# Optimization experiments

Measured on AMD Instinct MI355X. Metric: run time of the kernel, lower is better.

Reference implementation:

```python
import jax, jax.numpy as jnp
import numpy as np

B, L, D, H = 4, 2048, 1024, 16
DH = D // H


def setup_inputs() -> dict:
    key = jax.random.key(0)
    ks = jax.random.split(key, 16)
    s = 1.0 / np.sqrt(D)
    return {
        "query": jax.random.normal(ks[0], (B, L, D), jnp.float32),
        "key_": jax.random.normal(ks[1], (B, L, D), jnp.float32),
        "value": jax.random.normal(ks[2], (B, L, D), jnp.float32),
        "mask": jax.random.randint(ks[3], (B, L), 0, 2, jnp.int32),
        "Wq": jax.random.normal(ks[4], (D, D), jnp.float32) * s,
        "bq": jnp.zeros((D,), jnp.float32),
        "Wk": jax.random.normal(ks[5], (D, D), jnp.float32) * s,
        "bk": jnp.zeros((D,), jnp.float32),
        "Wv": jax.random.normal(ks[6], (D, D), jnp.float32) * s,
        "bv": jnp.zeros((D,), jnp.float32),
        "Wo": jax.random.normal(ks[7], (D, D), jnp.float32) * s,
        "bo": jnp.zeros((D,), jnp.float32),
        "gamma": jnp.ones((D,), jnp.float32),
        "beta": jnp.zeros((D,), jnp.float32),
    }


def reference(query, key_, value, mask, Wq, bq, Wk, bk, Wv, bv, Wo, bo, gamma, beta):
    old_query = query
    # projections (Linear: x @ W^T + b)
    q = query @ Wq.T + bq            # [B,L,D]
    k = key_ @ Wk.T + bk
    v = value @ Wv.T + bv
    # split heads -> [B,H,L,DH]
    q = q.reshape(B, L, H, DH).transpose(0, 2, 1, 3)
    k = k.reshape(B, L, H, DH).transpose(0, 2, 1, 3)
    v = v.reshape(B, L, H, DH).transpose(0, 2, 1, 3)
    scores = jnp.einsum("bhqd,bhkd->bhqk", q, k) / jnp.sqrt(jnp.float32(DH))
    m = mask[:, None, None, :]        # [B,1,1,L]
    scores = jnp.where(m == 0, jnp.float32(-1e9), scores)
    attn = jax.nn.softmax(scores, axis=-1)
    out = jnp.einsum("bhqk,bhkd->bhqd", attn, v)
    out = out.transpose(0, 2, 1, 3).reshape(B, L, D)
    out = out @ Wo.T + bo
    # dropout is identity in eval; residual + layernorm (eps=1e-5)
    x = out + old_query
    mu = jnp.mean(x, axis=-1, keepdims=True)
    var = jnp.var(x, axis=-1, keepdims=True)
    return (x - mu) / jnp.sqrt(var + 1e-5) * gamma + beta
```

## Files before the change

kernel.cpp:

```cpp
#include <hip/hip_runtime.h>
#include <hip/hip_bf16.h>

typedef __attribute__((ext_vector_type(4))) float f32x4;
typedef __attribute__((ext_vector_type(16))) float f32x16;
typedef __attribute__((ext_vector_type(2))) unsigned int u32x2;
typedef __attribute__((ext_vector_type(4))) unsigned int u32x4;
typedef __attribute__((ext_vector_type(8))) __bf16 bf16x8;

__device__ inline unsigned short f2bf(float x) {
    return __builtin_bit_cast(unsigned short, (__bf16)x);
}
__device__ inline unsigned int pack2(float lo, float hi) {
    return (unsigned int)f2bf(lo) | ((unsigned int)f2bf(hi) << 16);
}
__device__ inline u32x4 cvt8(const float* __restrict__ p) {
    f32x4 a = *(const f32x4*)p;
    f32x4 b = *(const f32x4*)(p + 4);
    u32x4 r;
    r[0] = pack2(a[0], a[1]);
    r[1] = pack2(a[2], a[3]);
    r[2] = pack2(b[0], b[1]);
    r[3] = pack2(b[2], b[3]);
    return r;
}
__device__ inline bf16x8 ldfrag(const unsigned short* p) {
    u32x4 t = *(const u32x4*)p;
    return __builtin_bit_cast(bf16x8, t);
}

__global__ __launch_bounds__(256) void cvt_bf16(
    const float* __restrict__ src, unsigned short* __restrict__ dst, int n8)
{
    for (int i = blockIdx.x * 256 + threadIdx.x; i < n8; i += gridDim.x * 256)
        *(u32x4*)(dst + (size_t)i * 8) = cvt8(src + (size_t)i * 8);
}
__global__ __launch_bounds__(256) void cvt_w3(
    const float* __restrict__ wq, const float* __restrict__ wk,
    const float* __restrict__ wv, unsigned short* __restrict__ dst)
{
    const float* s = blockIdx.y == 0 ? wq : (blockIdx.y == 1 ? wk : wv);
    unsigned short* d = dst + (size_t)blockIdx.y * 1048576;
    const int i = blockIdx.x * 256 + threadIdx.x;
    *(u32x4*)(d + (size_t)i * 8) = cvt8(s + (size_t)i * 8);
}

template<int MODE>
__global__ __launch_bounds__(256) void gemm_bt(
    const unsigned short* __restrict__ A, const unsigned short* __restrict__ Bw,
    const float* __restrict__ bias, const float* __restrict__ resid,
    void* __restrict__ Cp, float alpha)
{
    __shared__ unsigned short Al[2][128][32];
    __shared__ unsigned short Bl[2][128][32];
    const int tid = threadIdx.x;
    const int lane = tid & 63, w = tid >> 6;
    const int wr = w >> 1, wc = w & 1;
    const int m0 = blockIdx.x * 128, n0 = blockIdx.y * 128;
    const int fr = lane & 15, fq = lane >> 4;

    f32x4 acc[4][4] = {};

    auto stage = [&](int p, int k0) {
#pragma unroll
        for (int j = 0; j < 2; ++j) {
            const int f = (w * 2 + j) * 512 + lane * 8;
            const int r = f >> 5, c = f & 31;
            __builtin_amdgcn_global_load_lds(
                (const __attribute__((address_space(1))) void*)(A + (size_t)(m0 + r) * 1024 + k0 + c),
                (__attribute__((address_space(3))) void*)(&Al[p][0][0] + (w * 2 + j) * 512),
                16, 0, 0);
            __builtin_amdgcn_global_load_lds(
                (const __attribute__((address_space(1))) void*)(Bw + (size_t)(n0 + r) * 1024 + k0 + c),
                (__attribute__((address_space(3))) void*)(&Bl[p][0][0] + (w * 2 + j) * 512),
                16, 0, 0);
        }
    };

    stage(0, 0);
    __syncthreads();

    for (int k0 = 0; k0 < 1024; k0 += 32) {
        const int p = (k0 >> 5) & 1;
        if (k0 + 32 < 1024) stage(p ^ 1, k0 + 32);

        bf16x8 af[4], bfv[4];
#pragma unroll
        for (int mt = 0; mt < 4; ++mt)
            af[mt] = ldfrag(&Al[p][wr * 64 + mt * 16 + fr][8 * fq]);
#pragma unroll
        for (int nt = 0; nt < 4; ++nt)
            bfv[nt] = ldfrag(&Bl[p][wc * 64 + nt * 16 + fr][8 * fq]);
#pragma unroll
        for (int mt = 0; mt < 4; ++mt)
#pragma unroll
            for (int nt = 0; nt < 4; ++nt)
                acc[mt][nt] = __builtin_amdgcn_mfma_f32_16x16x32_bf16(af[mt], bfv[nt], acc[mt][nt], 0, 0, 0);
        __syncthreads();
    }

#pragma unroll
    for (int mt = 0; mt < 4; ++mt) {
#pragma unroll
        for (int nt = 0; nt < 4; ++nt) {
            const int col = n0 + wc * 64 + nt * 16 + fr;
            const float bb = bias[col];
            const int row0 = m0 + wr * 64 + mt * 16 + fq * 4;
            if (MODE == 2) {
                float v0 = acc[mt][nt][0] + bb, v1 = acc[mt][nt][1] + bb;
                float v2 = acc[mt][nt][2] + bb, v3 = acc[mt][nt][3] + bb;
                const int bb_ = row0 >> 11, key = row0 & 2047;
                const int key2 = (key & ~12) | ((key & 4) << 1) | ((key & 8) >> 1);
                const size_t idx = ((size_t)bb_ * 1024 + col) * 2048 + key2;
                u32x2 pv;
                pv[0] = pack2(v0, v1);
                pv[1] = pack2(v2, v3);
                *(u32x2*)((unsigned short*)Cp + idx) = pv;
            } else {
#pragma unroll
                for (int r = 0; r < 4; ++r) {
                    const size_t idx = (size_t)(row0 + r) * 1024 + col;
                    float v = (acc[mt][nt][r] + bb) * alpha;
                    if (MODE == 1) ((float*)Cp)[idx] = v + resid[idx];
                    else           ((unsigned short*)Cp)[idx] = f2bf(v);
                }
            }
        }
    }
}

__global__ __launch_bounds__(256, 2) void attn_fwd(
    const unsigned short* __restrict__ Q, const unsigned short* __restrict__ K,
    const unsigned short* __restrict__ Vt_g, const int* __restrict__ mask,
    unsigned short* __restrict__ O)
{
    __shared__ unsigned short Kl[2][64][64];
    __shared__ unsigned short Vl[2][64][64];
    __shared__ unsigned short mlb[2][64];
    const int tid = threadIdx.x, lane = tid & 63, w = tid >> 6;
    const int l31 = lane & 31, hi = lane >> 5;
    const int qb = blockIdx.y >> 3;
    const int bh = ((blockIdx.y & 7) << 3) | blockIdx.x;
    const int q0 = qb * 256;
    const int b = bh >> 4;
    const size_t rowbase = (size_t)b * 2048;
    const int hoff = (bh & 15) * 64;
    const size_t vbase = (size_t)bh * 64 * 2048;

    const u32x4 onesu = {0x3F803F80u, 0x3F803F80u, 0x3F803F80u, 0x3F803F80u};
    const bf16x8 vones = __builtin_bit_cast(bf16x8, onesu);

    const int sw0 = (((l31) ^ (l31 >> 3)) & 7) << 3;
    const int sw1 = (((l31) ^ ((l31 >> 3) + 4)) & 7) << 3;

    bf16x8 aq[2][4];
#pragma unroll
    for (int a = 0; a < 2; ++a) {
        const unsigned short* qp = Q + (rowbase + q0 + w * 64 + a * 32 + l31) * 1024 + hoff + hi * 8;
#pragma unroll
        for (int kk = 0; kk < 4; ++kk) aq[a][kk] = ldfrag(qp + kk * 16);
    }
    f32x16 o[2][2] = {};
    f32x16 os[2] = {};

    int srow[2], scol[2];
#pragma unroll
    for (int i = 0; i < 2; ++i) {
        int e = (i * 256 + tid) * 8;
        srow[i] = e >> 6;
        scol[i] = e & 63;
    }

    u32x4 kpre[2], vpre[2];
    int mpre = 0;
#pragma unroll
    for (int i = 0; i < 2; ++i) {
        kpre[i] = *(const u32x4*)(K + (rowbase + srow[i]) * 1024 + hoff + scol[i]);
        vpre[i] = *(const u32x4*)(Vt_g + vbase + (size_t)srow[i] * 2048 + scol[i]);
    }
    if (tid < 64) mpre = mask[rowbase + tid];

    for (int kb = 0, it = 0; kb < 2048; kb += 64, ++it) {
        const int p = it & 1;
#pragma unroll
        for (int i = 0; i < 2; ++i) {
            const int cs = scol[i] ^ (((srow[i] ^ (srow[i] >> 3)) & 7) << 3);
            *(u32x4*)&Kl[p][srow[i]][cs] = kpre[i];
            *(u32x4*)&Vl[p][srow[i]][cs] = vpre[i];
        }
        if (tid < 64) mlb[p][tid] = f2bf(mpre == 0 ? -30000.0f : 0.0f);
        if (kb + 64 < 2048) {
#pragma unroll
            for (int i = 0; i < 2; ++i) {
                kpre[i] = *(const u32x4*)(K + (rowbase + kb + 64 + srow[i]) * 1024 + hoff + scol[i]);
                vpre[i] = *(const u32x4*)(Vt_g + vbase + (size_t)srow[i] * 2048 + kb + 64 + scol[i]);
            }
            if (tid < 64) mpre = mask[rowbase + kb + 64 + tid];
        }
        __syncthreads();

#pragma unroll
        for (int t = 0; t < 2; ++t) {
            const int swt = t ? sw1 : sw0;
            const unsigned int mv = (hi == 0) ? (unsigned int)mlb[p][t * 32 + l31] : 0u;
            const u32x4 mfu = {mv, 0u, 0u, 0u};
            const bf16x8 kfm = __builtin_bit_cast(bf16x8, mfu);

            f32x16 z0 = {}, z1 = {};
            __builtin_amdgcn_s_setprio(1);
            z0 = __builtin_amdgcn_mfma_f32_32x32x16_bf16(kfm, vones, z0, 0, 0, 0);
            z1 = __builtin_amdgcn_mfma_f32_32x32x16_bf16(kfm, vones, z1, 0, 0, 0);
#pragma unroll
            for (int kk = 0; kk < 4; ++kk) {
                bf16x8 kf = ldfrag(&Kl[p][t * 32 + l31][(kk * 16 + hi * 8) ^ swt]);
                z0 = __builtin_amdgcn_mfma_f32_32x32x16_bf16(kf, aq[0][kk], z0, 0, 0, 0);
                z1 = __builtin_amdgcn_mfma_f32_32x32x16_bf16(kf, aq[1][kk], z1, 0, 0, 0);
            }
            __builtin_amdgcn_s_setprio(0);

            unsigned int pk[2][4][2];
#pragma unroll
            for (int g = 0; g < 4; ++g) {
                {
                    float p0 = __builtin_amdgcn_exp2f(z0[g * 4 + 0]);
                    float p1 = __builtin_amdgcn_exp2f(z0[g * 4 + 1]);
                    float p2 = __builtin_amdgcn_exp2f(z0[g * 4 + 2]);
                    float p3 = __builtin_amdgcn_exp2f(z0[g * 4 + 3]);
                    pk[0][g][0] = pack2(p0, p1);
                    pk[0][g][1] = pack2(p2, p3);
                }
                {
                    float p0 = __builtin_amdgcn_exp2f(z1[g * 4 + 0]);
                    float p1 = __builtin_amdgcn_exp2f(z1[g * 4 + 1]);
                    float p2 = __builtin_amdgcn_exp2f(z1[g * 4 + 2]);
                    float p3 = __builtin_amdgcn_exp2f(z1[g * 4 + 3]);
                    pk[1][g][0] = pack2(p0, p1);
                    pk[1][g][1] = pack2(p2, p3);
                }
            }

#pragma unroll
            for (int half = 0; half < 2; ++half) {
                const int c = t * 2 + half, G = half * 2;
                u32x4 fu0 = {pk[0][G][0], pk[0][G][1], pk[0][G + 1][0], pk[0][G + 1][1]};
                u32x4 fu1 = {pk[1][G][0], pk[1][G][1], pk[1][G + 1][0], pk[1][G + 1][1]};
                bf16x8 pf0 = __builtin_bit_cast(bf16x8, fu0);
                bf16x8 pf1 = __builtin_bit_cast(bf16x8, fu1);
                __builtin_amdgcn_s_setprio(1);
#pragma unroll
                for (int dt = 0; dt < 2; ++dt) {
                    const int swd = dt ? sw1 : sw0;
                    bf16x8 vb = ldfrag(&Vl[p][dt * 32 + l31][(c * 16 + hi * 8) ^ swd]);
                    o[0][dt] = __builtin_amdgcn_mfma_f32_32x32x16_bf16(pf0, vb, o[0][dt], 0, 0, 0);
                    o[1][dt] = __builtin_amdgcn_mfma_f32_32x32x16_bf16(pf1, vb, o[1][dt], 0, 0, 0);
                }
                os[0] = __builtin_amdgcn_mfma_f32_32x32x16_bf16(pf0, vones, os[0], 0, 0, 0);
                os[1] = __builtin_amdgcn_mfma_f32_32x32x16_bf16(pf1, vones, os[1], 0, 0, 0);
                __builtin_amdgcn_s_setprio(0);
            }
        }
    }

#pragma unroll
    for (int a = 0; a < 2; ++a)
#pragma unroll
        for (int g = 0; g < 4; ++g)
#pragma unroll
            for (int j = 0; j < 4; ++j) {
                const float inv = 1.0f / os[a][g * 4 + j];
                const size_t row = rowbase + q0 + w * 64 + a * 32 + g * 8 + hi * 4 + j;
#pragma unroll
                for (int dt = 0; dt < 2; ++dt)
                    O[row * 1024 + hoff + dt * 32 + l31] = f2bf(o[a][dt][g * 4 + j] * inv);
            }
}

__global__ __launch_bounds__(256) void ln_inplace(
    float* __restrict__ X, const float* __restrict__ gamma, const float* __restrict__ beta)
{
    __shared__ float red[8];
    const int tid = threadIdx.x, lane = tid & 63, w = tid >> 6;
    float* p = X + (size_t)blockIdx.x * 1024;
    f32x4 v = *((const f32x4*)p + tid);
    float s = v[0] + v[1] + v[2] + v[3];
    float s2 = v[0] * v[0] + v[1] * v[1] + v[2] * v[2] + v[3] * v[3];
#pragma unroll
    for (int d = 1; d < 64; d <<= 1) {
        s += __shfl_xor(s, d);
        s2 += __shfl_xor(s2, d);
    }
    if (lane == 0) { red[w] = s; red[4 + w] = s2; }
    __syncthreads();
    s = red[0] + red[1] + red[2] + red[3];
    s2 = red[4] + red[5] + red[6] + red[7];
    const float mu = s * (1.0f / 1024.0f);
    const float var = s2 * (1.0f / 1024.0f) - mu * mu;
    const float rstd = rsqrtf(var + 1e-5f);
    f32x4 g = *((const f32x4*)gamma + tid);
    f32x4 be = *((const f32x4*)beta + tid);
    f32x4 out;
#pragma unroll
    for (int j = 0; j < 4; ++j) out[j] = (v[j] - mu) * rstd * g[j] + be[j];
    *((f32x4*)p + tid) = out;
}

extern "C" void kernel_launch(void* const* d_in, const int* in_sizes, int n_in,
                              void* d_out, int out_size, void* d_ws, size_t ws_size,
                              hipStream_t stream) {
    const float* query = (const float*)d_in[0];
    const float* key_  = (const float*)d_in[1];
    const float* value = (const float*)d_in[2];
    const int*   mask  = (const int*)d_in[3];
    const float* Wq = (const float*)d_in[4];
    const float* bq = (const float*)d_in[5];
    const float* Wk = (const float*)d_in[6];
    const float* bk = (const float*)d_in[7];
    const float* Wv = (const float*)d_in[8];
    const float* bv = (const float*)d_in[9];
    const float* Wo = (const float*)d_in[10];
    const float* bo = (const float*)d_in[11];
    const float* gamma = (const float*)d_in[12];
    const float* beta  = (const float*)d_in[13];

    const size_t MD = (size_t)8192 * 1024;
    unsigned short* Qb  = (unsigned short*)d_ws;
    unsigned short* Kb  = Qb + MD;
    unsigned short* Vtb = Kb + MD;
    unsigned short* Ab  = Vtb + MD;
    float* out = (float*)d_out;
    unsigned short* W16 = (unsigned short*)d_out;
    unsigned short* Wo16 = Vtb;

    dim3 gg(64, 8);
    const float qscale = 0.125f * 1.4426950408889634f;

    cvt_w3<<<dim3(512, 3), 256, 0, stream>>>(Wq, Wk, Wv, W16);
    cvt_bf16<<<2048, 256, 0, stream>>>(query, Ab, 1048576);
    gemm_bt<0><<<gg, 256, 0, stream>>>(Ab, W16, bq, nullptr, Qb, qscale);
    cvt_bf16<<<2048, 256, 0, stream>>>(key_, Ab, 1048576);
    gemm_bt<0><<<gg, 256, 0, stream>>>(Ab, W16 + 1048576, bk, nullptr, Kb, 1.0f);
    cvt_bf16<<<2048, 256, 0, stream>>>(value, Ab, 1048576);
    gemm_bt<2><<<gg, 256, 0, stream>>>(Ab, W16 + 2097152, bv, nullptr, Vtb, 1.0f);

    attn_fwd<<<dim3(8, 64), 256, 0, stream>>>(Qb, Kb, Vtb, mask, Ab);

    cvt_bf16<<<512, 256, 0, stream>>>(Wo, Wo16, 131072);
    gemm_bt<1><<<gg, 256, 0, stream>>>(Ab, Wo16, bo, query, out, 1.0f);
    ln_inplace<<<8192, 256, 0, stream>>>(out, gamma, beta);
}
```

Baseline: 238.9 us.

## Fuse fp32-to-bf16 activation conversion into projection GEMMs and halve attention block size

The QKV projection GEMM now reads fp32 activations straight from global memory into registers, converts them to bf16 and stores them to padded LDS. This removes three separate conversion kernels and their round trip through the workspace. The GEMM and attention loops also move the barrier ahead of the next-tile prefetch, giving one sync per iteration. Attention blocks shrink to 128 threads covering 128 query rows, doubling the grid, which adds more K/V reloads per block. A risk is that register-staged A loads overlap less well than the previous direct-to-LDS loads.

```diff
diff --git a/kernel.cpp b/kernel.cpp
--- a/kernel.cpp
+++ b/kernel.cpp
@@ -44,13 +44,14 @@
     *(u32x4*)(d + (size_t)i * 8) = cvt8(s + (size_t)i * 8);
 }
 
-template<int MODE>
+template<bool AF32, int MODE>
 __global__ __launch_bounds__(256) void gemm_bt(
-    const unsigned short* __restrict__ A, const unsigned short* __restrict__ Bw,
+    const void* __restrict__ Ap, const unsigned short* __restrict__ Bw,
     const float* __restrict__ bias, const float* __restrict__ resid,
     void* __restrict__ Cp, float alpha)
 {
-    __shared__ unsigned short Al[2][128][32];
+    constexpr int ASTR = AF32 ? 40 : 32;
+    __shared__ unsigned short Al[2][128][ASTR];
     __shared__ unsigned short Bl[2][128][32];
     const int tid = threadIdx.x;
     const int lane = tid & 63, w = tid >> 6;
@@ -59,29 +60,65 @@
     const int fr = lane & 15, fq = lane >> 4;
 
     f32x4 acc[4][4] = {};
-
-    auto stage = [&](int p, int k0) {
+    f32x4 apre[2][2];
+
+    auto issueB = [&](int p, int k0) {
 #pragma unroll
         for (int j = 0; j < 2; ++j) {
             const int f = (w * 2 + j) * 512 + lane * 8;
             const int r = f >> 5, c = f & 31;
             __builtin_amdgcn_global_load_lds(
-                (const __attribute__((address_space(1))) void*)(A + (size_t)(m0 + r) * 1024 + k0 + c),
-                (__attribute__((address_space(3))) void*)(&Al[p][0][0] + (w * 2 + j) * 512),
-                16, 0, 0);
-            __builtin_amdgcn_global_load_lds(
                 (const __attribute__((address_space(1))) void*)(Bw + (size_t)(n0 + r) * 1024 + k0 + c),
                 (__attribute__((address_space(3))) void*)(&Bl[p][0][0] + (w * 2 + j) * 512),
                 16, 0, 0);
         }
     };
-
-    stage(0, 0);
-    __syncthreads();
+    auto issueA = [&](int p, int k0) {
+        if (AF32) {
+#pragma unroll
+            for (int i = 0; i < 2; ++i) {
+                const int e = (i * 256 + tid) * 8;
+                const int r = e >> 5, c = e & 31;
+                const float* src = (const float*)Ap + (size_t)(m0 + r) * 1024 + k0 + c;
+                apre[i][0] = *(const f32x4*)src;
+                apre[i][1] = *(const f32x4*)(src + 4);
+            }
+        } else {
+#pragma unroll
+            for (int j = 0; j < 2; ++j) {
+                const int f = (w * 2 + j) * 512 + lane * 8;
+                const int r = f >> 5, c = f & 31;
+                __builtin_amdgcn_global_load_lds(
+                    (const __attribute__((address_space(1))) void*)((const unsigned short*)Ap + (size_t)(m0 + r) * 1024 + k0 + c),
+                    (__attribute__((address_space(3))) void*)(&Al[p][0][0] + (w * 2 + j) * 512),
+                    16, 0, 0);
+            }
+        }
+    };
+
+    issueA(0, 0);
+    issueB(0, 0);
 
     for (int k0 = 0; k0 < 1024; k0 += 32) {
         const int p = (k0 >> 5) & 1;
-        if (k0 + 32 < 1024) stage(p ^ 1, k0 + 32);
+        if (AF32) {
+#pragma unroll
+            for (int i = 0; i < 2; ++i) {
+                const int e = (i * 256 + tid) * 8;
+                const int r = e >> 5, c = e & 31;
+                u32x4 v;
+                v[0] = pack2(apre[i][0][0], apre[i][0][1]);
+                v[1] = pack2(apre[i][0][2], apre[i][0][3]);
+                v[2] = pack2(apre[i][1][0], apre[i][1][1]);
+                v[3] = pack2(apre[i][1][2], apre[i][1][3]);
+                *(u32x4*)&Al[p][r][c] = v;
+            }
+        }
+        __syncthreads();
+        if (k0 + 32 < 1024) {
+            issueA(p ^ 1, k0 + 32);
+            issueB(p ^ 1, k0 + 32);
+        }
 
         bf16x8 af[4], bfv[4];
 #pragma unroll
@@ -95,7 +132,6 @@
 #pragma unroll
             for (int nt = 0; nt < 4; ++nt)
                 acc[mt][nt] = __builtin_amdgcn_mfma_f32_16x16x32_bf16(af[mt], bfv[nt], acc[mt][nt], 0, 0, 0);
-        __syncthreads();
     }
 
 #pragma unroll
@@ -128,7 +164,7 @@
     }
 }
 
-__global__ __launch_bounds__(256, 2) void attn_fwd(
+__global__ __launch_bounds__(128, 2) void attn_fwd(
     const unsigned short* __restrict__ Q, const unsigned short* __restrict__ K,
     const unsigned short* __restrict__ Vt_g, const int* __restrict__ mask,
     unsigned short* __restrict__ O)
@@ -140,7 +176,7 @@
     const int l31 = lane & 31, hi = lane >> 5;
     const int qb = blockIdx.y >> 3;
     const int bh = ((blockIdx.y & 7) << 3) | blockIdx.x;
-    const int q0 = qb * 256;
+    const int q0 = qb * 128;
     const int b = bh >> 4;
     const size_t rowbase = (size_t)b * 2048;
     const int hoff = (bh & 15) * 64;
@@ -162,18 +198,18 @@
     f32x16 o[2][2] = {};
     f32x16 os[2] = {};
 
-    int srow[2], scol[2];
-#pragma unroll
-    for (int i = 0; i < 2; ++i) {
-        int e = (i * 256 + tid) * 8;
+    int srow[4], scol[4];
+#pragma unroll
+    for (int i = 0; i < 4; ++i) {
+        int e = (i * 128 + tid) * 8;
         srow[i] = e >> 6;
         scol[i] = e & 63;
     }
 
-    u32x4 kpre[2], vpre[2];
+    u32x4 kpre[4], vpre[4];
     int mpre = 0;
 #pragma unroll
-    for (int i = 0; i < 2; ++i) {
+    for (int i = 0; i < 4; ++i) {
         kpre[i] = *(const u32x4*)(K + (rowbase + srow[i]) * 1024 + hoff + scol[i]);
         vpre[i] = *(const u32x4*)(Vt_g + vbase + (size_t)srow[i] * 2048 + scol[i]);
     }
@@ -182,21 +218,21 @@
     for (int kb = 0, it = 0; kb < 2048; kb += 64, ++it) {
         const int p = it & 1;
 #pragma unroll
-        for (int i = 0; i < 2; ++i) {
+        for (int i = 0; i < 4; ++i) {
             const int cs = scol[i] ^ (((srow[i] ^ (srow[i] >> 3)) & 7) << 3);
             *(u32x4*)&Kl[p][srow[i]][cs] = kpre[i];
             *(u32x4*)&Vl[p][srow[i]][cs] = vpre[i];
         }
         if (tid < 64) mlb[p][tid] = f2bf(mpre == 0 ? -30000.0f : 0.0f);
+        __syncthreads();
         if (kb + 64 < 2048) {
 #pragma unroll
-            for (int i = 0; i < 2; ++i) {
+            for (int i = 0; i < 4; ++i) {
                 kpre[i] = *(const u32x4*)(K + (rowbase + kb + 64 + srow[i]) * 1024 + hoff + scol[i]);
                 vpre[i] = *(const u32x4*)(Vt_g + vbase + (size_t)srow[i] * 2048 + kb + 64 + scol[i]);
             }
             if (tid < 64) mpre = mask[rowbase + kb + 64 + tid];
         }
-        __syncthreads();
 
 #pragma unroll
         for (int t = 0; t < 2; ++t) {
@@ -334,16 +370,13 @@
     const float qscale = 0.125f * 1.4426950408889634f;
 
     cvt_w3<<<dim3(512, 3), 256, 0, stream>>>(Wq, Wk, Wv, W16);
-    cvt_bf16<<<2048, 256, 0, stream>>>(query, Ab, 1048576);
-    gemm_bt<0><<<gg, 256, 0, stream>>>(Ab, W16, bq, nullptr, Qb, qscale);
-    cvt_bf16<<<2048, 256, 0, stream>>>(key_, Ab, 1048576);
-    gemm_bt<0><<<gg, 256, 0, stream>>>(Ab, W16 + 1048576, bk, nullptr, Kb, 1.0f);
-    cvt_bf16<<<2048, 256, 0, stream>>>(value, Ab, 1048576);
-    gemm_bt<2><<<gg, 256, 0, stream>>>(Ab, W16 + 2097152, bv, nullptr, Vtb, 1.0f);
-
-    attn_fwd<<<dim3(8, 64), 256, 0, stream>>>(Qb, Kb, Vtb, mask, Ab);
+    gemm_bt<true, 0><<<gg, 256, 0, stream>>>(query, W16,           bq, nullptr, Qb,  qscale);
+    gemm_bt<true, 0><<<gg, 256, 0, stream>>>(key_,  W16 + 1048576, bk, nullptr, Kb,  1.0f);
+    gemm_bt<true, 2><<<gg, 256, 0, stream>>>(value, W16 + 2097152, bv, nullptr, Vtb, 1.0f);
+
+    attn_fwd<<<dim3(8, 128), 128, 0, stream>>>(Qb, Kb, Vtb, mask, Ab);
 
     cvt_bf16<<<512, 256, 0, stream>>>(Wo, Wo16, 131072);
-    gemm_bt<1><<<gg, 256, 0, stream>>>(Ab, Wo16, bo, query, out, 1.0f);
+    gemm_bt<false, 1><<<gg, 256, 0, stream>>>(Ab, Wo16, bo, query, out, 1.0f);
     ln_inplace<<<8192, 256, 0, stream>>>(out, gamma, beta);
 }
```

Result: slower. 251.1 us (+5.1%).
